# Optimization experiments

Hardware: AMD Instinct MI355X
Metric: run time of the kernel (lower is better)

The kernel has to match this reference:

```python
import jax, jax.numpy as jnp
import numpy as np

B_IMG = 2
N_PROP = 2000
N_GT = 16
C_FEAT = 256
H_FEAT = 128
W_FEAT = 128
IMG = 1024.0
NUM_CLASSES = 2
BG_THRESH = 0.5          # fg==bg==0.5 -> BETWEEN_THRESHOLDS band is empty
BPI = 512                # batch_size_per_image
NUM_POS_MAX = int(BPI * 0.25)
ENC_W = (1.0, 1.0, 1.0, 1.0, 1.0)
SCALE = 1.0 / 8.0        # feature stride
POOL = 7
SR = 2                   # sampling_ratio
BETA = 1.0 / 9.0
HID = 1024


def _make_boxes(key, shape_prefix, img=IMG):
    kc, ks = jax.random.split(key)
    c = jax.random.uniform(kc, shape_prefix + (2,), minval=0.0, maxval=img)
    s = jax.random.uniform(ks, shape_prefix + (2,), minval=20.0, maxval=200.0)
    lo = jnp.clip(c - 0.5 * s, 0.0, img - 2.0)
    hi = jnp.clip(c + 0.5 * s, lo + 1.0, img)
    return jnp.concatenate([lo, hi], axis=-1)  # [.., x1,y1,x2,y2]


def setup_inputs():
    key = jax.random.key(0)
    ks = jax.random.split(key, 12)
    features = jax.random.normal(ks[0], (B_IMG, C_FEAT, H_FEAT, W_FEAT), dtype=jnp.float32)
    proposals = _make_boxes(ks[1], (B_IMG, N_PROP))
    gt_boxes = _make_boxes(ks[2], (B_IMG, N_GT))
    gt_labels = jax.random.randint(ks[3], (B_IMG, N_GT), 1, NUM_CLASSES, dtype=jnp.int32)
    ka, kb, kt = jax.random.split(ks[4], 3)
    a = jax.random.uniform(ka, (B_IMG, N_GT), minval=10.0, maxval=60.0)
    b = jax.random.uniform(kb, (B_IMG, N_GT), minval=5.0, maxval=30.0)
    th = jax.random.uniform(kt, (B_IMG, N_GT), minval=-np.pi / 2, maxval=np.pi / 2)
    exy = 0.5 * (gt_boxes[..., :2] + gt_boxes[..., 2:])
    gt_ellipses = jnp.stack([a, b, exy[..., 0], exy[..., 1], th], axis=-1)
    d_in = C_FEAT * POOL * POOL
    w1 = jax.random.normal(ks[5], (d_in, HID), dtype=jnp.float32) * 0.02
    b1 = jnp.zeros((HID,), jnp.float32)
    w2 = jax.random.normal(ks[6], (HID, HID), dtype=jnp.float32) * 0.02
    b2 = jnp.zeros((HID,), jnp.float32)
    wc = jax.random.normal(ks[7], (HID, NUM_CLASSES), dtype=jnp.float32) * 0.02
    bc = jnp.zeros((NUM_CLASSES,), jnp.float32)
    wr = jax.random.normal(ks[8], (HID, NUM_CLASSES * 6), dtype=jnp.float32) * 0.02
    br = jnp.zeros((NUM_CLASSES * 6,), jnp.float32)
    return dict(features=features, proposals=proposals, gt_boxes=gt_boxes,
                gt_labels=gt_labels, gt_ellipses=gt_ellipses,
                w1=w1, b1=b1, w2=w2, b2=b2, wc=wc, bc=bc, wr=wr, br=br)


def box_iou(b1, b2):  # [G,4], [P,4] -> [G,P]
    a1 = (b1[:, 2] - b1[:, 0]) * (b1[:, 3] - b1[:, 1])
    a2 = (b2[:, 2] - b2[:, 0]) * (b2[:, 3] - b2[:, 1])
    lt = jnp.maximum(b1[:, None, :2], b2[None, :, :2])
    rb = jnp.minimum(b1[:, None, 2:], b2[None, :, 2:])
    wh = jnp.clip(rb - lt, 0.0)
    inter = wh[..., 0] * wh[..., 1]
    return inter / (a1[:, None] + a2[None, :] - inter)


def encode_ellipses(ell, boxes):  # ell [..,5]=(a,b,cx,cy,theta), boxes [..,4] -> [..,6]
    a, b, ex, ey, th = (ell[..., i] for i in range(5))
    w = jnp.maximum(boxes[..., 2] - boxes[..., 0], 1.0)
    h = jnp.maximum(boxes[..., 3] - boxes[..., 1], 1.0)
    cx = 0.5 * (boxes[..., 0] + boxes[..., 2])
    cy = 0.5 * (boxes[..., 1] + boxes[..., 3])
    wx, wy, wa, wb, wt = ENC_W
    dx = wx * (ex - cx) / w
    dy = wy * (ey - cy) / h
    da = wa * jnp.log(jnp.maximum(2.0 * a, 1e-3) / w)
    db = wb * jnp.log(jnp.maximum(2.0 * b, 1e-3) / h)
    return jnp.stack([dx, dy, da, db, wt * jnp.sin(2.0 * th), wt * jnp.cos(2.0 * th)], axis=-1)


def roi_align(fmap, rois):  # [C,H,W], [R,4] -> [R,C,POOL,POOL]
    C, H, W = fmap.shape
    r = rois * SCALE
    x1, y1, x2, y2 = r[:, 0], r[:, 1], r[:, 2], r[:, 3]
    bw = jnp.maximum(x2 - x1, 1.0) / POOL
    bh = jnp.maximum(y2 - y1, 1.0) / POOL
    S = POOL * SR
    off = (jnp.arange(S, dtype=jnp.float32) + 0.5) / SR  # bin-unit sample offsets
    ys = jnp.clip(y1[:, None] + off[None, :] * bh[:, None], 0.0, H - 1.0)  # [R,S]
    xs = jnp.clip(x1[:, None] + off[None, :] * bw[:, None], 0.0, W - 1.0)
    y0 = jnp.clip(jnp.floor(ys), 0, H - 2).astype(jnp.int32)
    x0 = jnp.clip(jnp.floor(xs), 0, W - 2).astype(jnp.int32)
    ly = ys - y0
    lx = xs - x0
    Ya, Yb = y0[:, :, None], (y0 + 1)[:, :, None]  # [R,S,1]
    Xa, Xb = x0[:, None, :], (x0 + 1)[:, None, :]  # [R,1,S]
    v00 = fmap[:, Ya, Xa]; v01 = fmap[:, Ya, Xb]   # [C,R,S,S]
    v10 = fmap[:, Yb, Xa]; v11 = fmap[:, Yb, Xb]
    wy1 = ly[:, :, None]; wy0 = 1.0 - wy1
    wx1 = lx[:, None, :]; wx0 = 1.0 - wx1
    val = v00 * (wy0 * wx0) + v01 * (wy0 * wx1) + v10 * (wy1 * wx0) + v11 * (wy1 * wx1)
    R = rois.shape[0]
    pooled = val.reshape(C, R, POOL, SR, POOL, SR).mean(axis=(3, 5))
    return pooled.transpose(1, 0, 2, 3)


def reference(features, proposals, gt_boxes, gt_labels, gt_ellipses,
              w1, b1, w2, b2, wc, bc, wr, br):
    B = features.shape[0]
    # add_gt_proposals
    props = jnp.concatenate([proposals, gt_boxes], axis=1)            # [B,P,4]
    # assign_targets_to_proposals: IoU + Matcher (fg=bg=0.5)
    iou = jax.vmap(box_iou)(gt_boxes, props)                          # [B,G,P]
    matched_vals = iou.max(axis=1)
    matches = iou.argmax(axis=1)                                      # [B,P]
    lab = jnp.take_along_axis(gt_labels, matches, axis=1)
    lab = jnp.where(matched_vals < BG_THRESH, 0, lab)                 # background
    # BalancedPositiveNegativeSampler (deterministic, fixed-shape):
    # cap positives at NUM_POS_MAX by random rank, fill rest with random negatives
    rand = jax.random.uniform(jax.random.key(42), lab.shape)
    is_pos = lab > 0
    is_neg = lab == 0
    pos_s = jnp.where(is_pos, rand, -1e9)
    rank = jnp.argsort(jnp.argsort(-pos_s, axis=1), axis=1)
    capped = is_pos & (rank < NUM_POS_MAX)
    prio = jnp.where(capped, rand + 2.0, jnp.where(is_neg, rand, -1e9))
    _, idx = jax.lax.top_k(prio, BPI)                                 # [B,512]
    boxes = jnp.take_along_axis(props, idx[..., None], axis=1)        # [B,512,4]
    labels = jnp.take_along_axis(lab, idx, axis=1)                    # [B,512]
    m = jnp.take_along_axis(matches, idx, axis=1)
    ell = jnp.take_along_axis(gt_ellipses, m[..., None], axis=1)      # [B,512,5]
    targets = encode_ellipses(ell, boxes)                             # [B,512,6]
    # RoIAlign + TwoMLPHead + predictor
    pooled = jax.vmap(roi_align)(features, boxes)                     # [B,512,C,7,7]
    N = B * BPI
    x = pooled.reshape(N, -1)
    x = jax.nn.relu(x @ w1 + b1)
    x = jax.nn.relu(x @ w2 + b2)
    logits = x @ wc + bc                                              # [N,2]
    reg = (x @ wr + br).reshape(N, NUM_CLASSES, 6)
    # ellipse_rcnn_loss
    labels_f = labels.reshape(N)
    t = targets.reshape(N, 6)
    ce = -jnp.take_along_axis(jax.nn.log_softmax(logits, axis=-1), labels_f[:, None], axis=1).mean()
    pred = jnp.take_along_axis(reg, labels_f[:, None, None], axis=1)[:, 0]  # [N,6]
    d = jnp.abs(pred - t)
    sl1 = jnp.where(d < BETA, 0.5 * d * d / BETA, d - 0.5 * BETA)
    reg_loss = jnp.sum(sl1 * (labels_f > 0)[:, None].astype(sl1.dtype)) / N
    return jnp.stack([ce, reg_loss])
```

## Files before the change

kernel.cpp:

```cpp
#include <hip/hip_runtime.h>
#include <hip/hip_bf16.h>
#include <math.h>

#define B_IMG   2
#define N_PROP  2000
#define N_GT    16
#define NPROPS  2016
#define C_FEAT  256
#define H_FEAT  128
#define W_FEAT  128
#define HWF     (H_FEAT*W_FEAT)
#define POOL    7
#define BPI     512
#define NPOSMAX 128
#define NSEL    (B_IMG*BPI)
#define K1      (C_FEAT*POOL*POOL)
#define K1P     12800
#define HID     1024
#define NHEAD   14
#define SPLITK1 8

typedef short bf16x8f __attribute__((ext_vector_type(8)));
typedef float f32x4f  __attribute__((ext_vector_type(4)));
typedef short short4v __attribute__((ext_vector_type(4)));

__device__ __forceinline__ void threefry2x32(unsigned k0, unsigned k1,
                                             unsigned& x0, unsigned& x1) {
  unsigned ks[3] = {k0, k1, k0 ^ k1 ^ 0x1BD11BDAu};
  const int R0[4] = {13, 15, 26, 6};
  const int R1[4] = {17, 29, 16, 24};
  x0 += ks[0]; x1 += ks[1];
#pragma unroll
  for (int g = 0; g < 5; g++) {
    const int* rot = (g & 1) ? R1 : R0;
#pragma unroll
    for (int r = 0; r < 4; r++) {
      x0 += x1;
      x1 = (x1 << rot[r]) | (x1 >> (32 - rot[r]));
      x1 ^= x0;
    }
    x0 += ks[(g + 1) % 3];
    x1 += ks[(g + 2) % 3] + (unsigned)(g + 1);
  }
}

#define PRE_SAMPLE   2
#define PRE_TRANS    (PRE_SAMPLE + 2048)
#define PRE_CAST1    (PRE_TRANS + 3136)
#define PRE_CAST0    (PRE_CAST1 + 256)
#define PRE_TOTAL    (PRE_CAST0 + 512)

__global__ __launch_bounds__(256) void k_pre(const float* __restrict__ proposals,
                                             const float* __restrict__ gt_boxes,
                                             const int* __restrict__ gt_labels,
                                             const float* __restrict__ features,
                                             const float* __restrict__ w1,
                                             const float* __restrict__ w2,
                                             const float* __restrict__ gt_ell,
                                             __hip_bfloat16* __restrict__ featT,
                                             __hip_bfloat16* __restrict__ W1T,
                                             __hip_bfloat16* __restrict__ W2T,
                                             __hip_bfloat16* __restrict__ Xb,
                                             float* __restrict__ sel_boxes,
                                             int* __restrict__ sel_labels,
                                             float* __restrict__ targets) {
  __shared__ __align__(16) char smem[29056];
  int bid = blockIdx.x;
  int tid = threadIdx.x;
  if (bid < PRE_SAMPLE) {
    float* rs    = (float*)smem;
    int*   Hs    = (int*)(smem + 8064);
    int*   curs  = (int*)(smem + 8064 + 4112);
    float* pos_r = (float*)(smem + 8064);
    short* glist = (short*)(smem + 16272);
    short* pos_i = (short*)(smem + 16272);
    short* mt    = (short*)(smem + 20304);
    short* lbl   = (short*)(smem + 24336);
    float* gtb   = (float*)(smem + 28368);
    float* gte   = (float*)(smem + 28624);
    int*   gtl   = (int*)(smem + 28944);
    int*   cnt   = (int*)(smem + 29008);
    int b = bid;
    int base = b * NPROPS;
    if (tid == 0) *cnt = 0;
    if (tid < N_GT * 4) gtb[tid] = gt_boxes[b * N_GT * 4 + tid];
    if (tid < N_GT * 5) gte[tid] = gt_ell[b * N_GT * 5 + tid];
    if (tid < N_GT) gtl[tid] = gt_labels[b * N_GT + tid];
    __syncthreads();

    auto emitsel = [&](int slot, int i, int lab) {
      float p0, p1, p2, p3;
      if (i < N_PROP) {
        const float4 v = *(const float4*)(proposals + ((size_t)b * N_PROP + i) * 4);
        p0 = v.x; p1 = v.y; p2 = v.z; p3 = v.w;
      } else {
        const float* g = &gtb[(i - N_PROP) * 4];
        p0 = g[0]; p1 = g[1]; p2 = g[2]; p3 = g[3];
      }
      sel_boxes[slot * 4 + 0] = p0;
      sel_boxes[slot * 4 + 1] = p1;
      sel_boxes[slot * 4 + 2] = p2;
      sel_boxes[slot * 4 + 3] = p3;
      sel_labels[slot] = lab;
      const float* e = &gte[mt[i] * 5];
      float w = fmaxf(p2 - p0, 1.0f), h = fmaxf(p3 - p1, 1.0f);
      float cx = 0.5f * (p0 + p2), cy = 0.5f * (p1 + p3);
      float* t = targets + (size_t)slot * 6;
      t[0] = (e[2] - cx) / w;
      t[1] = (e[3] - cy) / h;
      t[2] = logf(fmaxf(2.0f * e[0], 0.001f) / w);
      t[3] = logf(fmaxf(2.0f * e[1], 0.001f) / h);
      t[4] = sinf(2.0f * e[4]);
      t[5] = cosf(2.0f * e[4]);
    };

    for (int i = tid; i < NPROPS; i += 256) {
      unsigned x0 = 0u, x1 = (unsigned)(base + i);
      threefry2x32(0u, 42u, x0, x1);
      unsigned bits = x0 ^ x1;
      float r = __uint_as_float((bits >> 9) | 0x3F800000u) - 1.0f;
      rs[i] = r;
      float p0, p1, p2, p3;
      if (i < N_PROP) {
        const float4 v = *(const float4*)(proposals + ((size_t)b * N_PROP + i) * 4);
        p0 = v.x; p1 = v.y; p2 = v.z; p3 = v.w;
      } else {
        const float* g = &gtb[(i - N_PROP) * 4];
        p0 = g[0]; p1 = g[1]; p2 = g[2]; p3 = g[3];
      }
      float a2 = (p2 - p0) * (p3 - p1);
      float best = -1.0f; int bg = 0;
#pragma unroll
      for (int g = 0; g < N_GT; g++) {
        float g0 = gtb[g*4], g1 = gtb[g*4+1], g2 = gtb[g*4+2], g3 = gtb[g*4+3];
        float a1 = (g2 - g0) * (g3 - g1);
        float wx = fmaxf(fminf(g2, p2) - fmaxf(g0, p0), 0.0f);
        float wy = fmaxf(fminf(g3, p3) - fmaxf(g1, p1), 0.0f);
        float inter = wx * wy;
        float iou = inter / (a1 + a2 - inter);
        if (iou > best) { best = iou; bg = g; }
      }
      mt[i] = (short)bg;
      int lab = (best < 0.5f) ? 0 : gtl[bg];
      lbl[i] = (short)lab;
      if (lab > 0) {
        int s = atomicAdd(cnt, 1);
        pos_i[s] = (short)i; pos_r[s] = r;
      }
    }
    __syncthreads();
    int P = *cnt;
    int Pp = (P < NPOSMAX) ? P : NPOSMAX;
    for (int s = tid; s < P; s += 256) {
      int i = pos_i[s]; float ri = pos_r[s];
      int ch = 0;
      for (int j = 0; j < P; j++) {
        float rj = pos_r[j]; int ij = pos_i[j];
        ch += (rj > ri || (rj == ri && ij < i)) ? 1 : 0;
      }
      if (ch < NPOSMAX) emitsel(b * BPI + ch, i, (int)lbl[i]);
    }
    __syncthreads();
    for (int idx = tid; idx < 1025; idx += 256) Hs[idx] = 0;
    __syncthreads();
    for (int i = tid; i < NPROPS; i += 256)
      if (lbl[i] == 0) {
        int bin = (int)(rs[i] * 1024.0f); if (bin > 1023) bin = 1023;
        atomicAdd(&Hs[bin], 1);
      }
    __syncthreads();
    for (int off = 1; off < 1024; off <<= 1) {
      int v[4];
#pragma unroll
      for (int k2 = 0; k2 < 4; k2++) {
        int idx = tid + k2 * 256;
        v[k2] = Hs[idx] + ((idx + off <= 1024) ? Hs[idx + off] : 0);
      }
      __syncthreads();
#pragma unroll
      for (int k2 = 0; k2 < 4; k2++) Hs[tid + k2 * 256] = v[k2];
      __syncthreads();
    }
    for (int idx = tid; idx < 1024; idx += 256) curs[idx] = 0;
    __syncthreads();
    for (int i = tid; i < NPROPS; i += 256)
      if (lbl[i] == 0) {
        int bin = (int)(rs[i] * 1024.0f); if (bin > 1023) bin = 1023;
        int o = atomicAdd(&curs[bin], 1);
        glist[Hs[bin + 1] + o] = (short)i;
      }
    __syncthreads();
    for (int i = tid; i < NPROPS; i += 256)
      if (lbl[i] == 0) {
        int bin = (int)(rs[i] * 1024.0f); if (bin > 1023) bin = 1023;
        int bbase = Hs[bin + 1];
        int cntb = Hs[bin] - bbase;
        float ri = rs[i];
        int wr = 0;
        for (int t = 0; t < cntb; t++) {
          int j = glist[bbase + t];
          if (j != i) {
            float rj = rs[j];
            wr += (rj > ri || (rj == ri && j < i)) ? 1 : 0;
          }
        }
        int slot = Pp + bbase + wr;
        if (slot < BPI) emitsel(b * BPI + slot, i, 0);
      }
  } else if (bid < PRE_TRANS) {
    float (*tile)[65] = (float(*)[65])smem;
    int t = bid - PRE_SAMPLE;
    int b = t >> 10;
    int rem = t & 1023;
    int c0 = (rem >> 8) * 64;
    int s0 = (rem & 255) * 64;
    const float* src = features + (size_t)b * C_FEAT * HWF;
    __hip_bfloat16* dst = featT + (size_t)b * HWF * C_FEAT;
    int hw4 = (tid & 15) * 4, cr = tid >> 4;
#pragma unroll
    for (int p = 0; p < 4; p++) {
      int c = cr + p * 16;
      float4 v = *(const float4*)(src + (size_t)(c0 + c) * HWF + s0 + hw4);
      tile[hw4 + 0][c] = v.x; tile[hw4 + 1][c] = v.y;
      tile[hw4 + 2][c] = v.z; tile[hw4 + 3][c] = v.w;
    }
    __syncthreads();
    int c4 = (tid & 15) * 4, hr = tid >> 4;
#pragma unroll
    for (int p = 0; p < 4; p++) {
      int hw = hr + p * 16;
      __hip_bfloat16 o[4] = {__float2bfloat16(tile[hw][c4]), __float2bfloat16(tile[hw][c4+1]),
                             __float2bfloat16(tile[hw][c4+2]), __float2bfloat16(tile[hw][c4+3])};
      *(short4v*)(dst + (size_t)(s0 + hw) * C_FEAT + c0 + c4) = *(short4v*)o;
    }
  } else if (bid < PRE_CAST1) {
    float (*tile)[65] = (float(*)[65])smem;
    int t = bid - PRE_TRANS;
    int p = t >> 6;
    int rem = t & 63;
    int c0 = (rem & 3) * 64;
    int n0 = (rem >> 2) * 64;
    int n4 = (tid & 15) * 4, ig = tid >> 4;
#pragma unroll
    for (int i = ig; i < 64; i += 16) {
      float4 v = *(const float4*)(w1 + (size_t)((c0 + i) * 49 + p) * HID + n0 + n4);
      tile[i][n4] = v.x; tile[i][n4 + 1] = v.y;
      tile[i][n4 + 2] = v.z; tile[i][n4 + 3] = v.w;
    }
    __syncthreads();
    int c4 = (tid & 15) * 4;
#pragma unroll
    for (int i = ig; i < 64; i += 16) {
      __hip_bfloat16 o[4] = {__float2bfloat16(tile[c4][i]), __float2bfloat16(tile[c4 + 1][i]),
                             __float2bfloat16(tile[c4 + 2][i]), __float2bfloat16(tile[c4 + 3][i])};
      *(short4v*)(W1T + (size_t)(n0 + i) * K1P + p * 256 + c0 + c4) = *(short4v*)o;
    }
  } else if (bid < PRE_CAST0) {
    float (*tile)[65] = (float(*)[65])smem;
    int t = bid - PRE_CAST1;
    int c0 = (t & 15) * 64;
    int n0 = (t >> 4) * 64;
    int n4 = (tid & 15) * 4, ig = tid >> 4;
#pragma unroll
    for (int i = ig; i < 64; i += 16) {
      float4 v = *(const float4*)(w2 + (size_t)(c0 + i) * HID + n0 + n4);
      tile[i][n4] = v.x; tile[i][n4 + 1] = v.y;
      tile[i][n4 + 2] = v.z; tile[i][n4 + 3] = v.w;
    }
    __syncthreads();
    int c4 = (tid & 15) * 4;
#pragma unroll
    for (int i = ig; i < 64; i += 16) {
      __hip_bfloat16 o[4] = {__float2bfloat16(tile[c4][i]), __float2bfloat16(tile[c4 + 1][i]),
                             __float2bfloat16(tile[c4 + 2][i]), __float2bfloat16(tile[c4 + 3][i])};
      *(short4v*)(W2T + (size_t)(n0 + i) * HID + c0 + c4) = *(short4v*)o;
    }
  } else {
    int t = bid - PRE_CAST0;
    __hip_bfloat16* buf = (t >> 8) ? W1T : Xb;
    int tt = (t & 255) * 256 + tid;
    int row = tt >> 6;
    int col4 = (tt & 63) << 2;
    short4v z = {0, 0, 0, 0};
    *(short4v*)(buf + (size_t)row * K1P + K1 + col4) = z;
  }
}

__global__ __launch_bounds__(256) void k_roialign(const __hip_bfloat16* __restrict__ featT,
                                                  const float* __restrict__ sel_boxes,
                                                  __hip_bfloat16* __restrict__ X) {
  int n = blockIdx.x;
  int py = blockIdx.y;
  int t = threadIdx.x;
  int px = t >> 5;
  int lane32 = t & 31;
  int c = lane32 << 3;
  int b = n >> 9;
  const float* bx = sel_boxes + (size_t)n * 4;
  float x1 = bx[0] * 0.125f, y1 = bx[1] * 0.125f;
  float x2 = bx[2] * 0.125f, y2 = bx[3] * 0.125f;
  float bw = fmaxf(x2 - x1, 1.0f) / 7.0f;
  float bh = fmaxf(y2 - y1, 1.0f) / 7.0f;
  if (px >= 7) return;
  const __hip_bfloat16* base = featT + (size_t)b * HWF * C_FEAT;
  int y0A[2]; float lyA[2];
#pragma unroll
  for (int sy = 0; sy < 2; sy++) {
    float off = ((float)(py * 2 + sy) + 0.5f) * 0.5f;
    float ys = fminf(fmaxf(y1 + off * bh, 0.0f), 127.0f);
    int y0 = (int)fminf(fmaxf(floorf(ys), 0.0f), 126.0f);
    y0A[sy] = y0; lyA[sy] = ys - (float)y0;
  }
  float acc[8] = {};
#pragma unroll
  for (int sx = 0; sx < 2; sx++) {
    float off = ((float)(px * 2 + sx) + 0.5f) * 0.5f;
    float xs = fminf(fmaxf(x1 + off * bw, 0.0f), 127.0f);
    int x0 = (int)fminf(fmaxf(floorf(xs), 0.0f), 126.0f);
    float lx = xs - (float)x0;
#pragma unroll
    for (int sy = 0; sy < 2; sy++) {
      int y0 = y0A[sy]; float ly = lyA[sy];
      const __hip_bfloat16* p = base + ((size_t)(y0 * W_FEAT + x0)) * C_FEAT + c;
      bf16x8f s00 = *(const bf16x8f*)p;
      bf16x8f s01 = *(const bf16x8f*)(p + C_FEAT);
      bf16x8f s10 = *(const bf16x8f*)(p + W_FEAT * C_FEAT);
      bf16x8f s11 = *(const bf16x8f*)(p + W_FEAT * C_FEAT + C_FEAT);
      float w00 = (1.0f - ly) * (1.0f - lx), w01 = (1.0f - ly) * lx;
      float w10 = ly * (1.0f - lx), w11 = ly * lx;
#pragma unroll
      for (int q = 0; q < 8; q++) {
        float v00 = __uint_as_float(((unsigned)(unsigned short)s00[q]) << 16);
        float v01 = __uint_as_float(((unsigned)(unsigned short)s01[q]) << 16);
        float v10 = __uint_as_float(((unsigned)(unsigned short)s10[q]) << 16);
        float v11 = __uint_as_float(((unsigned)(unsigned short)s11[q]) << 16);
        acc[q] += v00 * w00 + v01 * w01 + v10 * w10 + v11 * w11;
      }
    }
  }
  __hip_bfloat16 o[8];
#pragma unroll
  for (int q = 0; q < 8; q++) o[q] = __float2bfloat16(acc[q] * 0.25f);
  *(bf16x8f*)&X[(size_t)n * K1P + (size_t)(py * 7 + px) * C_FEAT + c] = *(bf16x8f*)o;
}

__device__ __forceinline__ void gld_lds16(const __hip_bfloat16* g, __hip_bfloat16* l) {
  __builtin_amdgcn_global_load_lds(
      (const __attribute__((address_space(1))) void*)g,
      (__attribute__((address_space(3))) void*)l, 16, 0, 0);
}

#define G1_KC   1600
#define G1_NKT  25
#define G1_ABUF 16384
#define G1_BUFE 24576

__global__ __launch_bounds__(512, 1) void k_gemm1(const __hip_bfloat16* __restrict__ A,
                                                  const __hip_bfloat16* __restrict__ BT,
                                                  __hip_bfloat16* __restrict__ Pb,
                                                  const float* __restrict__ b1,
                                                  __hip_bfloat16* __restrict__ H1b,
                                                  int* __restrict__ tile_cnt) {
  __shared__ __align__(16) __hip_bfloat16 lds[3 * G1_BUFE];
  __shared__ int lastf;
  const int lin = blockIdx.x;
  const int pair = (lin & 7) + ((lin >> 6) << 3);
  const int m0 = (pair & 3) * 256;
  const int kz = pair >> 2;
  const int n0 = ((lin >> 3) & 7) * 128;
  const int kbeg = kz * G1_KC;
  const int tid = threadIdx.x;
  const int wave = tid >> 6, lane = tid & 63;
  const int wm = (wave & 3) * 64, wn = (wave >> 2) * 64;
  const int lm = lane & 15, quad = lane >> 4;

  f32x4f acc[4][4] = {};

  auto stage = [&](int kt, int sb) {
    const int kcol = kbeg + kt * 64;
    __hip_bfloat16* lb = lds + sb * G1_BUFE;
#pragma unroll
    for (int u = 0; u < 4; ++u) {
      int idx = tid + u * 512;
      int r = idx >> 3, g = (idx & 7) ^ (r & 7);
      gld_lds16(A + (size_t)(m0 + r) * K1P + kcol + g * 8, lb + idx * 8);
    }
#pragma unroll
    for (int u = 0; u < 2; ++u) {
      int idx = tid + u * 512;
      int r = idx >> 3, g = (idx & 7) ^ (r & 7);
      gld_lds16(BT + (size_t)(n0 + r) * K1P + kcol + g * 8, lb + G1_ABUF + idx * 8);
    }
  };

  stage(0, 0);
  stage(1, 1);
  asm volatile("s_waitcnt vmcnt(6)" ::: "memory");
  __builtin_amdgcn_s_barrier();

  int buf = 0;
  for (int kt = 0; kt < G1_NKT; ++kt) {
    int sb = buf + 2; if (sb >= 3) sb -= 3;
    if (kt + 2 < G1_NKT) stage(kt + 2, sb);
    const __hip_bfloat16* Ab = lds + buf * G1_BUFE;
    const __hip_bfloat16* Bb = Ab + G1_ABUF;
    bf16x8f af[4][2], bf[4][2];
#pragma unroll
    for (int i = 0; i < 4; ++i)
#pragma unroll
      for (int s = 0; s < 2; ++s)
        af[i][s] = *(const bf16x8f*)(Ab + (wm + i * 16 + lm) * 64 +
                                     (((s << 2) + quad) ^ (lm & 7)) * 8);
#pragma unroll
    for (int j = 0; j < 4; ++j)
#pragma unroll
      for (int s = 0; s < 2; ++s)
        bf[j][s] = *(const bf16x8f*)(Bb + (wn + j * 16 + lm) * 64 +
                                     (((s << 2) + quad) ^ (lm & 7)) * 8);
    __builtin_amdgcn_s_setprio(1);
#pragma unroll
    for (int s = 0; s < 2; ++s)
#pragma unroll
      for (int i = 0; i < 4; ++i)
#pragma unroll
        for (int j = 0; j < 4; ++j)
          acc[i][j] = __builtin_amdgcn_mfma_f32_16x16x32_bf16(af[i][s], bf[j][s], acc[i][j], 0, 0, 0);
    __builtin_amdgcn_s_setprio(0);
    if (kt < G1_NKT - 1) {
      if (kt < G1_NKT - 2) asm volatile("s_waitcnt vmcnt(6)" ::: "memory");
      else                 asm volatile("s_waitcnt vmcnt(0)" ::: "memory");
      __builtin_amdgcn_s_barrier();
    }
    buf = (buf == 2) ? 0 : buf + 1;
  }

  const int tileid = (m0 >> 8) * 8 + (n0 >> 7);
  const int tileoff = tileid * 32768;
  __hip_bfloat16* dst = Pb + ((size_t)kz << 20) + tileoff + wave * 4096 + lane * 4;
#pragma unroll
  for (int i = 0; i < 4; ++i)
#pragma unroll
    for (int j = 0; j < 4; ++j) {
      __hip_bfloat16 o[4] = {__float2bfloat16(acc[i][j][0]), __float2bfloat16(acc[i][j][1]),
                             __float2bfloat16(acc[i][j][2]), __float2bfloat16(acc[i][j][3])};
      *(short4v*)(dst + (i * 4 + j) * 256) = *(short4v*)o;
    }
  __syncthreads();
  if (tid == 0) {
    __threadfence();
    int old = atomicAdd(&tile_cnt[tileid], 1);
    lastf = ((old & 7) == 7) ? 1 : 0;
  }
  __syncthreads();
  if (!lastf) return;
  __threadfence();
#pragma unroll
  for (int it = 0; it < 16; ++it) {
    int g = tid + it * 512;
    int eb = g * 4;
    int wv = eb >> 12, rem = eb & 4095;
    int fidx = rem >> 8, lanev = (rem & 255) >> 2;
    int qd = lanev >> 4, l = lanev & 15;
    int ii = fidx >> 2, jj = fidx & 3;
    int mrow = (wv & 3) * 64 + ii * 16 + qd * 4;
    int ncol = (wv >> 2) * 64 + jj * 16 + l;
    float s0 = 0.0f, s1 = 0.0f, s2 = 0.0f, s3 = 0.0f;
#pragma unroll
    for (int z = 0; z < SPLITK1; z++) {
      short4v v = *(const short4v*)(Pb + ((size_t)z << 20) + tileoff + eb);
      s0 += __uint_as_float(((unsigned)(unsigned short)v[0]) << 16);
      s1 += __uint_as_float(((unsigned)(unsigned short)v[1]) << 16);
      s2 += __uint_as_float(((unsigned)(unsigned short)v[2]) << 16);
      s3 += __uint_as_float(((unsigned)(unsigned short)v[3]) << 16);
    }
    float bv = b1[n0 + ncol];
    size_t ob = (size_t)(m0 + mrow) * HID + n0 + ncol;
    H1b[ob]            = __float2bfloat16(fmaxf(s0 + bv, 0.0f));
    H1b[ob + HID]      = __float2bfloat16(fmaxf(s1 + bv, 0.0f));
    H1b[ob + 2 * HID]  = __float2bfloat16(fmaxf(s2 + bv, 0.0f));
    H1b[ob + 3 * HID]  = __float2bfloat16(fmaxf(s3 + bv, 0.0f));
  }
}

#define G2_NKT  16
#define G2_ABUF 8192
#define G2_BUFE 16384
#define H2P     129

__global__ __launch_bounds__(512, 1) void k_gemm2h(const __hip_bfloat16* __restrict__ A,
                                                   const __hip_bfloat16* __restrict__ BT,
                                                   const float* __restrict__ b2,
                                                   const float* __restrict__ wc,
                                                   const float* __restrict__ wr,
                                                   float* __restrict__ Ypart,
                                                   const float* __restrict__ bc,
                                                   const float* __restrict__ br,
                                                   const int* __restrict__ sel_labels,
                                                   const float* __restrict__ T,
                                                   float* __restrict__ out,
                                                   int* __restrict__ loss_cnt) {
  __shared__ __align__(16) char smem[3 * G2_BUFE * 2];
  __shared__ int lastf;
  __hip_bfloat16* slds = (__hip_bfloat16*)smem;
  float* h2 = (float*)smem;
  float* wh = (float*)(smem + 128 * H2P * 4);
  const int m0 = (blockIdx.x >> 3) * 128;
  const int nb = blockIdx.x & 7;
  const int n0 = nb * 128;
  const int tid = threadIdx.x;
  const int wave = tid >> 6, lane = tid & 63;
  const int wm = (wave & 1) * 64, wn = (wave >> 1) * 32;
  const int lm = lane & 15, quad = lane >> 4;

  f32x4f acc[4][2] = {};

  auto stage = [&](int kt, int sb) {
    const int kcol = kt * 64;
    __hip_bfloat16* lb = slds + sb * G2_BUFE;
#pragma unroll
    for (int u = 0; u < 2; ++u) {
      int idx = tid + u * 512;
      int r = idx >> 3, g = (idx & 7) ^ (r & 7);
      gld_lds16(A + (size_t)(m0 + r) * HID + kcol + g * 8, lb + idx * 8);
    }
#pragma unroll
    for (int u = 0; u < 2; ++u) {
      int idx = tid + u * 512;
      int r = idx >> 3, g = (idx & 7) ^ (r & 7);
      gld_lds16(BT + (size_t)(n0 + r) * HID + kcol + g * 8, lb + G2_ABUF + idx * 8);
    }
  };

  stage(0, 0);
  stage(1, 1);
  asm volatile("s_waitcnt vmcnt(4)" ::: "memory");
  __builtin_amdgcn_s_barrier();

  int buf = 0;
  for (int kt = 0; kt < G2_NKT; ++kt) {
    int sb = buf + 2; if (sb >= 3) sb -= 3;
    if (kt + 2 < G2_NKT) stage(kt + 2, sb);
    const __hip_bfloat16* Ab = slds + buf * G2_BUFE;
    const __hip_bfloat16* Bb = Ab + G2_ABUF;
    bf16x8f af[4][2], bf[2][2];
#pragma unroll
    for (int i = 0; i < 4; ++i)
#pragma unroll
      for (int s = 0; s < 2; ++s)
        af[i][s] = *(const bf16x8f*)(Ab + (wm + i * 16 + lm) * 64 +
                                     (((s << 2) + quad) ^ (lm & 7)) * 8);
#pragma unroll
    for (int j = 0; j < 2; ++j)
#pragma unroll
      for (int s = 0; s < 2; ++s)
        bf[j][s] = *(const bf16x8f*)(Bb + (wn + j * 16 + lm) * 64 +
                                     (((s << 2) + quad) ^ (lm & 7)) * 8);
    __builtin_amdgcn_s_setprio(1);
#pragma unroll
    for (int s = 0; s < 2; ++s)
#pragma unroll
      for (int i = 0; i < 4; ++i)
#pragma unroll
        for (int j = 0; j < 2; ++j)
          acc[i][j] = __builtin_amdgcn_mfma_f32_16x16x32_bf16(af[i][s], bf[j][s], acc[i][j], 0, 0, 0);
    __builtin_amdgcn_s_setprio(0);
    if (kt < G2_NKT - 1) {
      if (kt < G2_NKT - 2) asm volatile("s_waitcnt vmcnt(4)" ::: "memory");
      else                 asm volatile("s_waitcnt vmcnt(0)" ::: "memory");
      __builtin_amdgcn_s_barrier();
    }
    buf = (buf == 2) ? 0 : buf + 1;
  }
  __syncthreads();

  float bb[2];
#pragma unroll
  for (int j = 0; j < 2; ++j) bb[j] = b2[n0 + wn + j * 16 + lm];
#pragma unroll
  for (int i = 0; i < 4; ++i)
#pragma unroll
    for (int j = 0; j < 2; ++j) {
      int col = wn + j * 16 + lm;
#pragma unroll
      for (int r = 0; r < 4; ++r) {
        int row = wm + i * 16 + quad * 4 + r;
        h2[row * H2P + col] = fmaxf(acc[i][j][r] + bb[j], 0.0f);
      }
    }
  for (int idx = tid; idx < 128 * 14; idx += 512) {
    int nl = idx / 14, j = idx - nl * 14;
    wh[idx] = (j < 2) ? wc[(size_t)(n0 + nl) * 2 + j]
                      : wr[(size_t)(n0 + nl) * 12 + (j - 2)];
  }
  __syncthreads();
  {
    int rrow = tid & 127, jg = tid >> 7;
    int j0 = jg * 4, jn = (jg == 3) ? 2 : 4;
    float s[4] = {};
#pragma unroll 4
    for (int k = 0; k < 128; ++k) {
      float h = h2[rrow * H2P + k];
      const float* w = wh + k * 14 + j0;
#pragma unroll
      for (int j = 0; j < 4; ++j) s[j] += h * w[j];
    }
    float* yp = Ypart + ((size_t)nb * NSEL + m0 + rrow) * 16 + j0;
    for (int j = 0; j < jn; ++j) yp[j] = s[j];
  }
  __syncthreads();
  if (tid == 0) {
    __threadfence();
    int old = atomicAdd(loss_cnt, 1);
    lastf = ((old & 63) == 63) ? 1 : 0;
  }
  __syncthreads();
  if (!lastf) return;
  __threadfence();
  float* sc = (float*)smem;
  float* sr = sc + 512;
  float ce_s = 0.0f, rg_s = 0.0f;
#pragma unroll
  for (int half = 0; half < 2; ++half) {
    int n = tid + half * 512;
    float y[14];
#pragma unroll
    for (int j = 0; j < 14; ++j) y[j] = (j < 2) ? bc[j] : br[j - 2];
#pragma unroll
    for (int nb2 = 0; nb2 < 8; ++nb2) {
      const float* p = Ypart + ((size_t)nb2 * NSEL + n) * 16;
      float4 v0 = *(const float4*)(p + 0);
      float4 v1 = *(const float4*)(p + 4);
      float4 v2 = *(const float4*)(p + 8);
      float2 v3 = *(const float2*)(p + 12);
      y[0] += v0.x; y[1] += v0.y; y[2] += v0.z; y[3] += v0.w;
      y[4] += v1.x; y[5] += v1.y; y[6] += v1.z; y[7] += v1.w;
      y[8] += v2.x; y[9] += v2.y; y[10] += v2.z; y[11] += v2.w;
      y[12] += v3.x; y[13] += v3.y;
    }
    int lb = sel_labels[n];
    float mx = fmaxf(y[0], y[1]);
    float lse = mx + logf(expf(y[0] - mx) + expf(y[1] - mx));
    ce_s += lse - (lb ? y[1] : y[0]);
    if (lb > 0) {
      const float beta = 1.0f / 9.0f;
      const float* t = T + (size_t)n * 6;
#pragma unroll
      for (int j = 0; j < 6; j++) {
        float d = fabsf(y[2 + lb * 6 + j] - t[j]);
        rg_s += (d < beta) ? (0.5f * d * d / beta) : (d - 0.5f * beta);
      }
    }
  }
  sc[tid] = ce_s; sr[tid] = rg_s;
  __syncthreads();
  for (int sft = 256; sft > 0; sft >>= 1) {
    if (tid < sft) { sc[tid] += sc[tid + sft]; sr[tid] += sr[tid + sft]; }
    __syncthreads();
  }
  if (tid == 0) {
    out[0] = sc[0] * (1.0f / 1024.0f);
    out[1] = sr[0] * (1.0f / 1024.0f);
  }
}

extern "C" void kernel_launch(void* const* d_in, const int* in_sizes, int n_in,
                              void* d_out, int out_size, void* d_ws, size_t ws_size,
                              hipStream_t stream) {
  const float* features  = (const float*)d_in[0];
  const float* proposals = (const float*)d_in[1];
  const float* gt_boxes  = (const float*)d_in[2];
  const int*   gt_labels = (const int*)d_in[3];
  const float* gt_ell    = (const float*)d_in[4];
  const float* w1 = (const float*)d_in[5];
  const float* b1 = (const float*)d_in[6];
  const float* w2 = (const float*)d_in[7];
  const float* b2 = (const float*)d_in[8];
  const float* wc = (const float*)d_in[9];
  const float* bc = (const float*)d_in[10];
  const float* wr = (const float*)d_in[11];
  const float* br = (const float*)d_in[12];
  float* out = (float*)d_out;

  char* ws = (char*)d_ws;
  size_t off = 0;
  auto take = [&](size_t bytes) -> void* {
    void* p = ws + off;
    off = (off + bytes + 255) & ~(size_t)255;
    return p;
  };
  __hip_bfloat16* Pb = (__hip_bfloat16*)take((size_t)16 * (1 << 20) * 2);
  __hip_bfloat16* featT = Pb;
  __hip_bfloat16* Xb  = (__hip_bfloat16*)take((size_t)NSEL * K1P * 2);
  __hip_bfloat16* W1T = (__hip_bfloat16*)take((size_t)HID * K1P * 2);
  __hip_bfloat16* W2T = (__hip_bfloat16*)take((size_t)HID * HID * 2);
  __hip_bfloat16* H1b = (__hip_bfloat16*)take((size_t)NSEL * HID * 2);
  float* Ypart     = (float*)take((size_t)8 * NSEL * 16 * 4);
  float* sel_boxes = (float*)take((size_t)NSEL * 4 * 4);
  int*   sel_lab   = (int*)take((size_t)NSEL * 4);
  float* targets   = (float*)take((size_t)NSEL * 6 * 4);
  int*   loss_cnt  = (int*)take(256);
  int*   tile_cnt  = (int*)take(256);

  k_pre<<<PRE_TOTAL, 256, 0, stream>>>(proposals, gt_boxes, gt_labels, features,
                                       w1, w2, gt_ell, featT, W1T, W2T, Xb,
                                       sel_boxes, sel_lab, targets);
  k_roialign<<<dim3(NSEL, POOL), 256, 0, stream>>>(featT, sel_boxes, Xb);

  k_gemm1<<<256, 512, 0, stream>>>(Xb, W1T, Pb, b1, H1b, tile_cnt);
  k_gemm2h<<<64, 512, 0, stream>>>(H1b, W2T, b2, wc, wr, Ypart,
                                   bc, br, sel_lab, targets, out, loss_cnt);
}
```

Before: 270.3 us.

## Replace pipelined split-K GEMM1 with simple 128x128 kernel plus separate reduce

```diff
diff --git a/kernel.cpp b/kernel.cpp
--- a/kernel.cpp
+++ b/kernel.cpp
@@ -19,6 +19,7 @@
 #define HID     1024
 #define NHEAD   14
 #define SPLITK1 8
+#define G1_KC   1600
 
 typedef short bf16x8f __attribute__((ext_vector_type(8)));
 typedef float f32x4f  __attribute__((ext_vector_type(4)));
@@ -350,136 +351,85 @@
       (__attribute__((address_space(3))) void*)l, 16, 0, 0);
 }
 
-#define G1_KC   1600
-#define G1_NKT  25
-#define G1_ABUF 16384
-#define G1_BUFE 24576
-
-__global__ __launch_bounds__(512, 1) void k_gemm1(const __hip_bfloat16* __restrict__ A,
-                                                  const __hip_bfloat16* __restrict__ BT,
-                                                  __hip_bfloat16* __restrict__ Pb,
-                                                  const float* __restrict__ b1,
-                                                  __hip_bfloat16* __restrict__ H1b,
-                                                  int* __restrict__ tile_cnt) {
-  __shared__ __align__(16) __hip_bfloat16 lds[3 * G1_BUFE];
-  __shared__ int lastf;
-  const int lin = blockIdx.x;
-  const int pair = (lin & 7) + ((lin >> 6) << 3);
-  const int m0 = (pair & 3) * 256;
-  const int kz = pair >> 2;
-  const int n0 = ((lin >> 3) & 7) * 128;
-  const int kbeg = kz * G1_KC;
-  const int tid = threadIdx.x;
-  const int wave = tid >> 6, lane = tid & 63;
-  const int wm = (wave & 3) * 64, wn = (wave >> 2) * 64;
-  const int lm = lane & 15, quad = lane >> 4;
-
+__global__ __launch_bounds__(256) void k_gemm1s(const __hip_bfloat16* __restrict__ A,
+                                                const __hip_bfloat16* __restrict__ BT,
+                                                __hip_bfloat16* __restrict__ Pb) {
+  __shared__ __align__(16) __hip_bfloat16 As[128 * 32];
+  __shared__ __align__(16) __hip_bfloat16 Bs[128 * 32];
+  int lin = blockIdx.x;
+  int kz = lin & 7;
+  int q  = lin >> 3;
+  int n0 = (q & 7) * 128;
+  int m0 = (q >> 3) * 128;
+  int tid = threadIdx.x;
+  int kbeg = kz * G1_KC;
+  int srow = tid >> 2;
+  int scs  = tid & 3;
+  int sg   = scs ^ (srow & 3);
+  int scol = sg << 3;
+  int wave = tid >> 6, lane = tid & 63;
+  int wm = (wave & 1) * 64, wn = (wave >> 1) * 64;
+  int lm = lane & 15, quad = lane >> 4;
+  int fco = ((quad ^ (lm & 3)) << 3);
   f32x4f acc[4][4] = {};
-
-  auto stage = [&](int kt, int sb) {
-    const int kcol = kbeg + kt * 64;
-    __hip_bfloat16* lb = lds + sb * G1_BUFE;
-#pragma unroll
-    for (int u = 0; u < 4; ++u) {
-      int idx = tid + u * 512;
-      int r = idx >> 3, g = (idx & 7) ^ (r & 7);
-      gld_lds16(A + (size_t)(m0 + r) * K1P + kcol + g * 8, lb + idx * 8);
-    }
-#pragma unroll
-    for (int u = 0; u < 2; ++u) {
-      int idx = tid + u * 512;
-      int r = idx >> 3, g = (idx & 7) ^ (r & 7);
-      gld_lds16(BT + (size_t)(n0 + r) * K1P + kcol + g * 8, lb + G1_ABUF + idx * 8);
-    }
-  };
-
-  stage(0, 0);
-  stage(1, 1);
-  asm volatile("s_waitcnt vmcnt(6)" ::: "memory");
-  __builtin_amdgcn_s_barrier();
-
-  int buf = 0;
-  for (int kt = 0; kt < G1_NKT; ++kt) {
-    int sb = buf + 2; if (sb >= 3) sb -= 3;
-    if (kt + 2 < G1_NKT) stage(kt + 2, sb);
-    const __hip_bfloat16* Ab = lds + buf * G1_BUFE;
-    const __hip_bfloat16* Bb = Ab + G1_ABUF;
-    bf16x8f af[4][2], bf[4][2];
-#pragma unroll
-    for (int i = 0; i < 4; ++i)
-#pragma unroll
-      for (int s = 0; s < 2; ++s)
-        af[i][s] = *(const bf16x8f*)(Ab + (wm + i * 16 + lm) * 64 +
-                                     (((s << 2) + quad) ^ (lm & 7)) * 8);
-#pragma unroll
-    for (int j = 0; j < 4; ++j)
-#pragma unroll
-      for (int s = 0; s < 2; ++s)
-        bf[j][s] = *(const bf16x8f*)(Bb + (wn + j * 16 + lm) * 64 +
-                                     (((s << 2) + quad) ^ (lm & 7)) * 8);
-    __builtin_amdgcn_s_setprio(1);
-#pragma unroll
-    for (int s = 0; s < 2; ++s)
-#pragma unroll
-      for (int i = 0; i < 4; ++i)
-#pragma unroll
-        for (int j = 0; j < 4; ++j)
-          acc[i][j] = __builtin_amdgcn_mfma_f32_16x16x32_bf16(af[i][s], bf[j][s], acc[i][j], 0, 0, 0);
-    __builtin_amdgcn_s_setprio(0);
-    if (kt < G1_NKT - 1) {
-      if (kt < G1_NKT - 2) asm volatile("s_waitcnt vmcnt(6)" ::: "memory");
-      else                 asm volatile("s_waitcnt vmcnt(0)" ::: "memory");
-      __builtin_amdgcn_s_barrier();
-    }
-    buf = (buf == 2) ? 0 : buf + 1;
-  }
-
-  const int tileid = (m0 >> 8) * 8 + (n0 >> 7);
-  const int tileoff = tileid * 32768;
+  for (int k0 = kbeg; k0 < kbeg + G1_KC; k0 += 32) {
+    __syncthreads();
+#pragma unroll
+    for (int r0 = 0; r0 < 128; r0 += 64)
+      gld_lds16(A + (size_t)(m0 + r0 + srow) * K1P + k0 + scol, &As[(r0 + srow) * 32 + scs * 8]);
+#pragma unroll
+    for (int r0 = 0; r0 < 128; r0 += 64)
+      gld_lds16(BT + (size_t)(n0 + r0 + srow) * K1P + k0 + scol, &Bs[(r0 + srow) * 32 + scs * 8]);
+    __syncthreads();
+    bf16x8f af[4], bf[4];
+#pragma unroll
+    for (int i = 0; i < 4; i++)
+      af[i] = *(const bf16x8f*)&As[(wm + i * 16 + lm) * 32 + fco];
+#pragma unroll
+    for (int j = 0; j < 4; j++)
+      bf[j] = *(const bf16x8f*)&Bs[(wn + j * 16 + lm) * 32 + fco];
+#pragma unroll
+    for (int i = 0; i < 4; i++)
+#pragma unroll
+      for (int j = 0; j < 4; j++)
+        acc[i][j] = __builtin_amdgcn_mfma_f32_16x16x32_bf16(af[i], bf[j], acc[i][j], 0, 0, 0);
+  }
+  int tileoff = ((m0 >> 7) * 8 + (n0 >> 7)) * 16384;
   __hip_bfloat16* dst = Pb + ((size_t)kz << 20) + tileoff + wave * 4096 + lane * 4;
 #pragma unroll
-  for (int i = 0; i < 4; ++i)
-#pragma unroll
-    for (int j = 0; j < 4; ++j) {
+  for (int i = 0; i < 4; i++)
+#pragma unroll
+    for (int j = 0; j < 4; j++) {
       __hip_bfloat16 o[4] = {__float2bfloat16(acc[i][j][0]), __float2bfloat16(acc[i][j][1]),
                              __float2bfloat16(acc[i][j][2]), __float2bfloat16(acc[i][j][3])};
       *(short4v*)(dst + (i * 4 + j) * 256) = *(short4v*)o;
     }
-  __syncthreads();
-  if (tid == 0) {
-    __threadfence();
-    int old = atomicAdd(&tile_cnt[tileid], 1);
-    lastf = ((old & 7) == 7) ? 1 : 0;
-  }
-  __syncthreads();
-  if (!lastf) return;
-  __threadfence();
-#pragma unroll
-  for (int it = 0; it < 16; ++it) {
-    int g = tid + it * 512;
-    int eb = g * 4;
-    int wv = eb >> 12, rem = eb & 4095;
-    int fidx = rem >> 8, lanev = (rem & 255) >> 2;
-    int qd = lanev >> 4, l = lanev & 15;
-    int ii = fidx >> 2, jj = fidx & 3;
-    int mrow = (wv & 3) * 64 + ii * 16 + qd * 4;
-    int ncol = (wv >> 2) * 64 + jj * 16 + l;
-    float s0 = 0.0f, s1 = 0.0f, s2 = 0.0f, s3 = 0.0f;
-#pragma unroll
-    for (int z = 0; z < SPLITK1; z++) {
-      short4v v = *(const short4v*)(Pb + ((size_t)z << 20) + tileoff + eb);
-      s0 += __uint_as_float(((unsigned)(unsigned short)v[0]) << 16);
-      s1 += __uint_as_float(((unsigned)(unsigned short)v[1]) << 16);
-      s2 += __uint_as_float(((unsigned)(unsigned short)v[2]) << 16);
-      s3 += __uint_as_float(((unsigned)(unsigned short)v[3]) << 16);
-    }
-    float bv = b1[n0 + ncol];
-    size_t ob = (size_t)(m0 + mrow) * HID + n0 + ncol;
-    H1b[ob]            = __float2bfloat16(fmaxf(s0 + bv, 0.0f));
-    H1b[ob + HID]      = __float2bfloat16(fmaxf(s1 + bv, 0.0f));
-    H1b[ob + 2 * HID]  = __float2bfloat16(fmaxf(s2 + bv, 0.0f));
-    H1b[ob + 3 * HID]  = __float2bfloat16(fmaxf(s3 + bv, 0.0f));
-  }
+}
+
+__global__ __launch_bounds__(256) void k_reduce16(const __hip_bfloat16* __restrict__ Pb,
+                                                  const float* __restrict__ bias,
+                                                  __hip_bfloat16* __restrict__ O) {
+  int m4 = blockIdx.x >> 2;
+  int n  = (blockIdx.x & 3) * 256 + threadIdx.x;
+  int m0i = m4 >> 5, wavem = (m4 >> 4) & 1, i = (m4 >> 2) & 3, quad = m4 & 3;
+  int n0i = n >> 7, wn_i = (n >> 6) & 1, j = (n >> 4) & 3, lm = n & 15;
+  int wave = wavem + wn_i * 2;
+  int elem = (m0i * 8 + n0i) * 16384 + wave * 4096 + (i * 4 + j) * 256 + (quad * 16 + lm) * 4;
+  float s0 = 0.0f, s1 = 0.0f, s2 = 0.0f, s3 = 0.0f;
+#pragma unroll
+  for (int z = 0; z < SPLITK1; z++) {
+    short4v v = *(const short4v*)(Pb + ((size_t)z << 20) + elem);
+    s0 += __uint_as_float(((unsigned)(unsigned short)v[0]) << 16);
+    s1 += __uint_as_float(((unsigned)(unsigned short)v[1]) << 16);
+    s2 += __uint_as_float(((unsigned)(unsigned short)v[2]) << 16);
+    s3 += __uint_as_float(((unsigned)(unsigned short)v[3]) << 16);
+  }
+  float bv = bias[n];
+  int m = m4 * 4;
+  O[(size_t)(m + 0) * HID + n] = __float2bfloat16(fmaxf(s0 + bv, 0.0f));
+  O[(size_t)(m + 1) * HID + n] = __float2bfloat16(fmaxf(s1 + bv, 0.0f));
+  O[(size_t)(m + 2) * HID + n] = __float2bfloat16(fmaxf(s2 + bv, 0.0f));
+  O[(size_t)(m + 3) * HID + n] = __float2bfloat16(fmaxf(s3 + bv, 0.0f));
 }
 
 #define G2_NKT  16
@@ -699,14 +649,14 @@
   int*   sel_lab   = (int*)take((size_t)NSEL * 4);
   float* targets   = (float*)take((size_t)NSEL * 6 * 4);
   int*   loss_cnt  = (int*)take(256);
-  int*   tile_cnt  = (int*)take(256);
 
   k_pre<<<PRE_TOTAL, 256, 0, stream>>>(proposals, gt_boxes, gt_labels, features,
                                        w1, w2, gt_ell, featT, W1T, W2T, Xb,
                                        sel_boxes, sel_lab, targets);
   k_roialign<<<dim3(NSEL, POOL), 256, 0, stream>>>(featT, sel_boxes, Xb);
 
-  k_gemm1<<<256, 512, 0, stream>>>(Xb, W1T, Pb, b1, H1b, tile_cnt);
+  k_gemm1s<<<512, 256, 0, stream>>>(Xb, W1T, Pb);
+  k_reduce16<<<1024, 256, 0, stream>>>(Pb, b1, H1b);
   k_gemm2h<<<64, 512, 0, stream>>>(H1b, W2T, b2, wc, wr, Ypart,
                                    bc, br, sel_lab, targets, out, loss_cnt);
 }
```

Result: faster. 250.6 us (-7.3%).
